# Performance work log

Measured on AMD Instinct MI355X. Metric: run time of the kernel, lower is better.

Reference implementation:

```python
import jax, jax.numpy as jnp
import numpy as np

WINDOW_SIZE = 11
SIGMA = 1.5
C1 = 0.01 ** 2
C2 = 0.03 ** 2


def _gaussian_window(window_size, sigma):
    coords = jnp.arange(window_size, dtype=jnp.float32) - window_size // 2
    g = jnp.exp(-coords ** 2 / (2 * sigma ** 2))
    g = g / g.sum()
    w = g[None, :] * g[:, None]           # [K, K]
    return w[None, None, :, :]            # [1, 1, K, K] (OIHW)


def _conv_same(x, window):
    # x: [B, 1, H, W], window: [1, 1, K, K]; padding = K//2 (SAME for odd K)
    p = WINDOW_SIZE // 2
    return jax.lax.conv_general_dilated(
        x, window, window_strides=(1, 1), padding=[(p, p), (p, p)],
        dimension_numbers=("NCHW", "OIHW", "NCHW"))


def setup_inputs() -> dict:
    key = jax.random.key(0)
    k1, k2 = jax.random.split(key)
    pred = jax.random.uniform(k1, (32, 3, 512, 512), dtype=jnp.float32)
    target = jax.random.uniform(k2, (32, 3, 512, 512), dtype=jnp.float32)
    window = _gaussian_window(WINDOW_SIZE, SIGMA)
    return {"pred": pred, "target": target, "window": window}


def reference(pred, target, window):
    # channel-mean to single channel if C > 1
    if pred.shape[1] > 1:
        pred = jnp.mean(pred, axis=1, keepdims=True)
    if target.shape[1] > 1:
        target = jnp.mean(target, axis=1, keepdims=True)

    mu1 = _conv_same(pred, window)
    mu2 = _conv_same(target, window)
    mu1_sq = mu1 ** 2
    mu2_sq = mu2 ** 2
    mu1_mu2 = mu1 * mu2
    sigma1_sq = _conv_same(pred * pred, window) - mu1_sq
    sigma2_sq = _conv_same(target * target, window) - mu2_sq
    sigma12 = _conv_same(pred * target, window) - mu1_mu2

    ssim_map = ((2 * mu1_mu2 + C1) * (2 * sigma12 + C2)) / (
        (mu1_sq + mu2_sq + C1) * (sigma1_sq + sigma2_sq + C2))
    return jnp.mean(1.0 - ssim_map)
```

## Files before the change

### kernel.cpp

```cpp
#include <hip/hip_runtime.h>


typedef float f32x2 __attribute__((ext_vector_type(2)));

constexpr int KW   = 11;
constexpr int HALF = 5;
constexpr int IMG_H = 512;
constexpr int IMG_W = 512;
constexpr int NB   = 32;
constexpr int NCH  = 3;
constexpr int TR   = 32;
constexpr int BT   = 512;
constexpr int LW   = IMG_W + 16;
constexpr int NP   = (TR + 2 * HALF) / 2;

__global__ __launch_bounds__(BT)
void ssim_fused(const float* __restrict__ pred,
                const float* __restrict__ targ,
                const float* __restrict__ win,
                float* __restrict__ out)
{
    __shared__ f32x2 lds[2][2][LW];
    __shared__ float red[BT / 64];

    const int tid  = threadIdx.x;
    const int nrow = IMG_H / TR;
    const int img  = blockIdx.x / nrow;
    const int R0   = (blockIdx.x % nrow) * TR;

    if (tid < 64) {
        int b = tid & 1, r = (tid >> 1) & 1, s = (tid >> 2) & 1, k = tid >> 3;
        int idx = s ? (IMG_W + 8 + k) : k;
        lds[b][r][idx] = (f32x2)(0.f, 0.f);
    }

    float gs[6];
    {
        float g5 = sqrtf(win[HALF * KW + HALF]);
        #pragma unroll
        for (int j = 0; j < 6; ++j) gs[j] = win[HALF * KW + j] / g5;
    }
    auto W = [&](int j) { return gs[j <= 5 ? j : 10 - j]; };

    const size_t ims = (size_t)IMG_H * IMG_W;
    const int hpos    = tid & 255;
    const int row_off = tid >> 8;
    const float* pb = pred + (size_t)img * NCH * ims + (size_t)hpos * 2;
    const float* tb = targ + (size_t)img * NCH * ims + (size_t)hpos * 2;
    const float inv3 = 1.0f / 3.0f;

    float2 p0, p1, p2, t0, t1, t2;
    auto issue = [&](int pair) {
        int r = R0 - HALF + 2 * pair + row_off;
        if (r >= 0 && r < IMG_H) {
            const float* pr = pb + (size_t)r * IMG_W;
            const float* tr = tb + (size_t)r * IMG_W;
            p0 = *(const float2*)(pr);
            p1 = *(const float2*)(pr + ims);
            p2 = *(const float2*)(pr + 2 * ims);
            t0 = *(const float2*)(tr);
            t1 = *(const float2*)(tr + ims);
            t2 = *(const float2*)(tr + 2 * ims);
        } else {
            p0 = make_float2(0.f, 0.f);
            p1 = p0; p2 = p0; t0 = p0; t1 = p0; t2 = p0;
        }
    };
    auto commit = [&](int pair) {
        float4 m;
        m.x = (p0.x + p1.x + p2.x) * inv3;
        m.y = (t0.x + t1.x + t2.x) * inv3;
        m.z = (p0.y + p1.y + p2.y) * inv3;
        m.w = (t0.y + t1.y + t2.y) * inv3;
        *(float4*)&lds[pair & 1][row_off][8 + 2 * hpos] = m;
    };

    f32x2 rMU[12], rSQ[12];
    float rPT[12];
    #pragma unroll
    for (int k = 0; k < 12; ++k) {
        rMU[k] = (f32x2)(0.f, 0.f); rSQ[k] = (f32x2)(0.f, 0.f); rPT[k] = 0.f;
    }

    const float C1 = 1e-4f, C2 = 9e-4f;
    const int c = tid;
    float acc = 0.f;

    issue(0);
    for (int i = 0; i < NP; ++i) {
        commit(i);
        if (i + 1 < NP) issue(i + 1);
        __syncthreads();
        const int buf = i & 1;

        #pragma unroll
        for (int rr = 0; rr < 2; ++rr) {
            f32x2 mu = (f32x2)(0.f, 0.f), sq = (f32x2)(0.f, 0.f);
            float spt = 0.f;
            #pragma unroll
            for (int j = 0; j < KW; ++j) {
                const float w = W(j);
                f32x2 v = lds[buf][rr][c + 3 + j];
                mu  += v * w;
                sq  += (v * v) * w;
                spt += (v.x * v.y) * w;
            }
            rMU[10 + rr] = mu; rSQ[10 + rr] = sq; rPT[10 + rr] = spt;
        }

        if (i >= 5) {
            #pragma unroll
            for (int off = 0; off < 2; ++off) {
                f32x2 m = (f32x2)(0.f, 0.f), e = (f32x2)(0.f, 0.f);
                float ept = 0.f;
                #pragma unroll
                for (int k = 0; k < KW; ++k) {
                    const float w = W(k);
                    m += rMU[off + k] * w;
                    e += rSQ[off + k] * w;
                    ept += rPT[off + k] * w;
                }
                f32x2 msq = m * m;
                float m12 = m.x * m.y;
                f32x2 s = e - msq;
                float s12 = ept - m12;
                float num = (2.f * m12 + C1) * (2.f * s12 + C2);
                float den = (msq.x + msq.y + C1) * (s.x + s.y + C2);
                acc += 1.f - num * __builtin_amdgcn_rcpf(den);
            }
        }

        #pragma unroll
        for (int k = 0; k < 10; ++k) {
            rMU[k] = rMU[k + 2]; rSQ[k] = rSQ[k + 2]; rPT[k] = rPT[k + 2];
        }
    }

    #pragma unroll
    for (int off = 32; off >= 1; off >>= 1)
        acc += __shfl_down(acc, off, 64);
    if ((tid & 63) == 0) red[tid >> 6] = acc;
    __syncthreads();
    if (tid == 0) {
        float s = 0.f;
        #pragma unroll
        for (int w = 0; w < BT / 64; ++w) s += red[w];
        atomicAdd(out, s * (1.0f / ((float)NB * IMG_H * IMG_W)));
    }
}

extern "C" void kernel_launch(void* const* d_in, const int* in_sizes, int n_in,
                              void* d_out, int out_size, void* d_ws, size_t ws_size,
                              hipStream_t stream) {
    const float* pred = (const float*)d_in[0];
    const float* targ = (const float*)d_in[1];
    const float* win  = (const float*)d_in[2];
    float* out = (float*)d_out;

    hipMemsetAsync(out, 0, sizeof(float), stream);

    dim3 grid(NB * (IMG_H / TR));
    ssim_fused<<<grid, BT, 0, stream>>>(pred, targ, win, out);
}
```

Before: 95.32 us.

## Give each wavefront its own 64x16 tile and drop block barriers

Work moves from 512-thread blocks covering full-width 32-row strips to independent per-wavefront tiles of 64 columns by 16 rows. Each wave keeps a private LDS line buffer, and __syncthreads is replaced by wave-local fences. This is meant to remove block-wide barrier stalls and raise the number of independent units in flight. The cost is halo overhead: 10 extra columns and 10 extra rows per 64x16 tile mean more redundant loads and more vertical-convolution warmup, plus scalar uncoalesced-ish loads instead of float2.

```diff
diff --git a/kernel.cpp b/kernel.cpp
--- a/kernel.cpp
+++ b/kernel.cpp
@@ -2,6 +2,10 @@
 
 
 typedef float f32x2 __attribute__((ext_vector_type(2)));
+
+static __device__ __forceinline__ f32x2 mk2(float x, float y) {
+    f32x2 r; r.x = x; r.y = y; return r;
+}
 
 constexpr int KW   = 11;
 constexpr int HALF = 5;
@@ -9,10 +13,12 @@
 constexpr int IMG_W = 512;
 constexpr int NB   = 32;
 constexpr int NCH  = 3;
-constexpr int TR   = 32;
-constexpr int BT   = 512;
-constexpr int LW   = IMG_W + 16;
-constexpr int NP   = (TR + 2 * HALF) / 2;
+constexpr int TCW  = 64;
+constexpr int TRW  = 16;
+constexpr int NP   = (TRW + 2*HALF) / 2;
+constexpr int WPB  = 4;
+constexpr int BT   = WPB * 64;
+constexpr int LSLOT = 80;
 
 __global__ __launch_bounds__(BT)
 void ssim_fused(const float* __restrict__ pred,
@@ -20,98 +26,100 @@
                 const float* __restrict__ win,
                 float* __restrict__ out)
 {
-    __shared__ f32x2 lds[2][2][LW];
-    __shared__ float red[BT / 64];
+    __shared__ f32x2 lbuf[WPB][2][LSLOT];
+    __shared__ float red[WPB];
 
     const int tid  = threadIdx.x;
-    const int nrow = IMG_H / TR;
-    const int img  = blockIdx.x / nrow;
-    const int R0   = (blockIdx.x % nrow) * TR;
-
-    if (tid < 64) {
-        int b = tid & 1, r = (tid >> 1) & 1, s = (tid >> 2) & 1, k = tid >> 3;
-        int idx = s ? (IMG_W + 8 + k) : k;
-        lds[b][r][idx] = (f32x2)(0.f, 0.f);
-    }
+    const int lane = tid & 63;
+    const int wid  = tid >> 6;
+    const int gw   = blockIdx.x * WPB + wid;
+    const int ct   = gw & 7;
+    const int st   = (gw >> 3) & 31;
+    const int img  = gw >> 8;
+    const int c0   = ct * TCW;
+    const int R0   = st * TRW;
 
     float gs[6];
     {
-        float g5 = sqrtf(win[HALF * KW + HALF]);
+        float g5 = sqrtf(win[HALF*KW + HALF]);
         #pragma unroll
-        for (int j = 0; j < 6; ++j) gs[j] = win[HALF * KW + j] / g5;
+        for (int j = 0; j < 6; ++j) gs[j] = win[HALF*KW + j] / g5;
     }
     auto W = [&](int j) { return gs[j <= 5 ? j : 10 - j]; };
 
     const size_t ims = (size_t)IMG_H * IMG_W;
-    const int hpos    = tid & 255;
-    const int row_off = tid >> 8;
-    const float* pb = pred + (size_t)img * NCH * ims + (size_t)hpos * 2;
-    const float* tb = targ + (size_t)img * NCH * ims + (size_t)hpos * 2;
-    const float inv3 = 1.0f / 3.0f;
+    const float* pb = pred + (size_t)img * NCH * ims;
+    const float* tb = targ + (size_t)img * NCH * ims;
 
-    float2 p0, p1, p2, t0, t1, t2;
-    auto issue = [&](int pair) {
-        int r = R0 - HALF + 2 * pair + row_off;
-        if (r >= 0 && r < IMG_H) {
-            const float* pr = pb + (size_t)r * IMG_W;
-            const float* tr = tb + (size_t)r * IMG_W;
-            p0 = *(const float2*)(pr);
-            p1 = *(const float2*)(pr + ims);
-            p2 = *(const float2*)(pr + 2 * ims);
-            t0 = *(const float2*)(tr);
-            t1 = *(const float2*)(tr + ims);
-            t2 = *(const float2*)(tr + 2 * ims);
+    const int cm  = c0 - HALF + lane;
+    const int chc = c0 + 59 + lane;
+    const bool okm = (unsigned)cm  < (unsigned)IMG_W;
+    const bool okh = (lane < 10) && ((unsigned)chc < (unsigned)IMG_W);
+
+    float a0,a1,a2,b0,b1,b2;
+    float e0,e1,e2,e3,e4,e5;
+    auto issue = [&](int rowidx) {
+        int r = R0 - HALF + rowidx;
+        if ((unsigned)r < (unsigned)IMG_H) {
+            size_t base = (size_t)r * IMG_W;
+            if (okm) { size_t a = base + cm;
+                a0=pb[a]; a1=pb[a+ims]; a2=pb[a+2*ims];
+                b0=tb[a]; b1=tb[a+ims]; b2=tb[a+2*ims];
+            } else { a0=a1=a2=b0=b1=b2=0.f; }
+            if (okh) { size_t a = base + chc;
+                e0=pb[a]; e1=pb[a+ims]; e2=pb[a+2*ims];
+                e3=tb[a]; e4=tb[a+ims]; e5=tb[a+2*ims];
+            } else { e0=e1=e2=e3=e4=e5=0.f; }
         } else {
-            p0 = make_float2(0.f, 0.f);
-            p1 = p0; p2 = p0; t0 = p0; t1 = p0; t2 = p0;
+            a0=a1=a2=b0=b1=b2=0.f;
+            e0=e1=e2=e3=e4=e5=0.f;
         }
     };
-    auto commit = [&](int pair) {
-        float4 m;
-        m.x = (p0.x + p1.x + p2.x) * inv3;
-        m.y = (t0.x + t1.x + t2.x) * inv3;
-        m.z = (p0.y + p1.y + p2.y) * inv3;
-        m.w = (t0.y + t1.y + t2.y) * inv3;
-        *(float4*)&lds[pair & 1][row_off][8 + 2 * hpos] = m;
+    const float inv3 = 1.f/3.f;
+    auto commit = [&](int slot) {
+        lbuf[wid][slot][lane] = mk2((a0+a1+a2)*inv3, (b0+b1+b2)*inv3);
+        if (lane < 10)
+            lbuf[wid][slot][64+lane] = mk2((e0+e1+e2)*inv3, (e3+e4+e5)*inv3);
     };
 
     f32x2 rMU[12], rSQ[12];
     float rPT[12];
     #pragma unroll
     for (int k = 0; k < 12; ++k) {
-        rMU[k] = (f32x2)(0.f, 0.f); rSQ[k] = (f32x2)(0.f, 0.f); rPT[k] = 0.f;
+        rMU[k] = mk2(0.f, 0.f); rSQ[k] = mk2(0.f, 0.f); rPT[k] = 0.f;
     }
 
+    auto hconv = [&](int slot, f32x2& oMU, f32x2& oSQ, float& oPT) {
+        const f32x2* Lr = &lbuf[wid][slot][lane];
+        f32x2 mu = mk2(0.f, 0.f), sq = mk2(0.f, 0.f);
+        float pt = 0.f;
+        #pragma unroll
+        for (int j = 0; j < KW; ++j) {
+            const float w = W(j);
+            f32x2 v = Lr[j];
+            mu += v * w; sq += (v * v) * w; pt += (v.x * v.y) * w;
+        }
+        oMU = mu; oSQ = sq; oPT = pt;
+    };
+
     const float C1 = 1e-4f, C2 = 9e-4f;
-    const int c = tid;
     float acc = 0.f;
 
     issue(0);
     for (int i = 0; i < NP; ++i) {
-        commit(i);
-        if (i + 1 < NP) issue(i + 1);
-        __syncthreads();
-        const int buf = i & 1;
-
-        #pragma unroll
-        for (int rr = 0; rr < 2; ++rr) {
-            f32x2 mu = (f32x2)(0.f, 0.f), sq = (f32x2)(0.f, 0.f);
-            float spt = 0.f;
-            #pragma unroll
-            for (int j = 0; j < KW; ++j) {
-                const float w = W(j);
-                f32x2 v = lds[buf][rr][c + 3 + j];
-                mu  += v * w;
-                sq  += (v * v) * w;
-                spt += (v.x * v.y) * w;
-            }
-            rMU[10 + rr] = mu; rSQ[10 + rr] = sq; rPT[10 + rr] = spt;
-        }
+        commit(0);
+        __threadfence_block();
+        issue(2*i + 1);
+        hconv(0, rMU[10], rSQ[10], rPT[10]);
+        commit(1);
+        __threadfence_block();
+        if (i + 1 < NP) issue(2*i + 2);
+        hconv(1, rMU[11], rSQ[11], rPT[11]);
 
         if (i >= 5) {
             #pragma unroll
             for (int off = 0; off < 2; ++off) {
-                f32x2 m = (f32x2)(0.f, 0.f), e = (f32x2)(0.f, 0.f);
+                f32x2 m = mk2(0.f, 0.f), e = mk2(0.f, 0.f);
                 float ept = 0.f;
                 #pragma unroll
                 for (int k = 0; k < KW; ++k) {
@@ -139,12 +147,12 @@
     #pragma unroll
     for (int off = 32; off >= 1; off >>= 1)
         acc += __shfl_down(acc, off, 64);
-    if ((tid & 63) == 0) red[tid >> 6] = acc;
+    if (lane == 0) red[wid] = acc;
     __syncthreads();
     if (tid == 0) {
         float s = 0.f;
         #pragma unroll
-        for (int w = 0; w < BT / 64; ++w) s += red[w];
+        for (int w = 0; w < WPB; ++w) s += red[w];
         atomicAdd(out, s * (1.0f / ((float)NB * IMG_H * IMG_W)));
     }
 }
@@ -159,6 +167,6 @@
 
     hipMemsetAsync(out, 0, sizeof(float), stream);
 
-    dim3 grid(NB * (IMG_H / TR));
+    dim3 grid((NB * 32 * 8) / WPB);
     ssim_fused<<<grid, BT, 0, stream>>>(pred, targ, win, out);
 }
```

Result: slower. 148.4 us (+55.7%).
